# Optimization experiments

Measured on AMD Instinct MI355X. Metric: run time of the kernel, lower is better.

## Reference

```python
import jax, jax.numpy as jnp
import numpy as np

B, N, D = 2, 2048, 1024
H = 16
HD = D // H  # 64
NEG = -1e30


def setup_inputs() -> dict:
    key = jax.random.key(0)
    ks = jax.random.split(key, 6)
    s = 0.02
    return {
        "x": jax.random.normal(ks[0], (B, N, D), dtype=jnp.float32),
        "Wq": jax.random.normal(ks[1], (D, D), dtype=jnp.float32) * s,
        "Wk": jax.random.normal(ks[2], (D, D), dtype=jnp.float32) * s,
        "Wv": jax.random.normal(ks[3], (D, D), dtype=jnp.float32) * s,
        "Wo": jax.random.normal(ks[4], (D, D), dtype=jnp.float32) * s,
        "Wf": jax.random.normal(ks[5], (D, H), dtype=jnp.float32) * s,
    }


def reference(x, Wq, Wk, Wv, Wo, Wf):
    b, n, d = x.shape
    h, hd = H, HD
    scale = hd ** -0.5
    # projections (Linear without bias; weights stored as [in, out])
    q = (x @ Wq).reshape(b, n, h, hd).transpose(0, 2, 1, 3)  # b h n hd
    k = (x @ Wk).reshape(b, n, h, hd).transpose(0, 2, 1, 3)
    v = (x @ Wv).reshape(b, n, h, hd).transpose(0, 2, 1, 3)
    # per-head log forget gate, cumulative sum over positions
    log_f = jax.nn.log_sigmoid(x @ Wf).transpose(0, 2, 1)  # b h n
    c = jnp.cumsum(log_f, axis=-1)  # b h n
    # scores with additive decay bias: bias[i,j] = c[i] - c[j] (j <= i)
    scores = jnp.einsum('bhid,bhjd->bhij', q, k) * scale
    scores = scores + c[..., :, None] - c[..., None, :]
    causal = jnp.tril(jnp.ones((n, n), dtype=bool))
    scores = jnp.where(causal, scores, NEG)
    attn = jax.nn.softmax(scores, axis=-1)
    out = jnp.einsum('bhij,bhjd->bhid', attn, v)  # b h n hd
    out = out.transpose(0, 2, 1, 3).reshape(b, n, d)
    return out @ Wo
```

## Files before the change

### kernel.cpp

```cpp
#include <hip/hip_runtime.h>
#include <hip/hip_bf16.h>
#include <stdint.h>

#define NN 2048
#define DD 1024
#define HH 16
#define HDD 64
#define QBLK 64
#define KVBLK 128

typedef unsigned short u16;
typedef __attribute__((ext_vector_type(8))) __bf16 bf16x8_t;
typedef __attribute__((ext_vector_type(4))) float f32x4_t;

#define LOG2E 1.44269504f

static __device__ __forceinline__ u16 f2bf(float f) {
  union { float f; uint32_t u; } v; v.f = f;
  uint32_t r = v.u + 0x7FFFu + ((v.u >> 16) & 1u);
  return (u16)(r >> 16);
}

static __device__ __forceinline__ uint32_t packbf2(float a, float b) {
  __hip_bfloat162 h2 = __float22bfloat162_rn(make_float2(a, b));
  union { __hip_bfloat162 hh; uint32_t u; } cvt; cvt.hh = h2;
  return cvt.u;
}

static __device__ __forceinline__ float exp2_raw(float x) {
  float r;
  asm("v_exp_f32 %0, %1" : "=v"(r) : "v"(x));
  return r;
}

static __device__ __forceinline__ void async_copy16(const void* g, void* l) {
  __builtin_amdgcn_global_load_lds((const __attribute__((address_space(1))) void*)g,
                                   (__attribute__((address_space(3))) void*)l, 16, 0, 0);
}

__global__ void prep_kernel(const float* __restrict__ x, const float* __restrict__ Wf,
                            float* __restrict__ lf, u16* __restrict__ xb,
                            const float* __restrict__ W0, const float* __restrict__ W1,
                            const float* __restrict__ W2, const float* __restrict__ W3,
                            u16* __restrict__ Wt) {
  __shared__ float xs[DD];
  __shared__ float part[16][17];
  __shared__ float tile[64][65];
  int t = threadIdx.x;
  if (blockIdx.x < 4096) {
    int row = blockIdx.x;
    float4 v = *(const float4*)&x[(size_t)row * DD + t * 4];
    *(float4*)&xs[t * 4] = v;
    ushort4 o;
    o.x = f2bf(v.x); o.y = f2bf(v.y); o.z = f2bf(v.z); o.w = f2bf(v.w);
    *(ushort4*)&xb[(size_t)row * DD + t * 4] = o;
    __syncthreads();
    int h = t & 15, chunk = t >> 4;
    float s = 0.f;
#pragma unroll 8
    for (int e = 0; e < 64; e++)
      s += xs[chunk * 64 + e] * Wf[(chunk * 64 + e) * HH + h];
    part[chunk][h] = s;
    __syncthreads();
    if (t < 16) {
      float z = 0.f;
#pragma unroll
      for (int i = 0; i < 16; i++) z += part[i][t];
      float ls = fminf(z, 0.f) - log1pf(__expf(-fabsf(z)));
      int b = row >> 11, n = row & (NN - 1);
      lf[(b * HH + t) * NN + n] = ls;
    }
  } else {
    int bid = blockIdx.x - 4096;
    int wq = bid >> 8;
    const float* W = wq == 0 ? W0 : wq == 1 ? W1 : wq == 2 ? W2 : W3;
    u16* out = Wt + (size_t)wq * DD * DD;
    int bx = bid & 15;
    int by = (bid >> 4) & 15;
    int c = t & 63, r4 = t >> 6;
#pragma unroll
    for (int i = 0; i < 16; i++) {
      int row = i * 4 + r4;
      tile[row][c] = W[(by * 64 + row) * DD + bx * 64 + c];
    }
    __syncthreads();
#pragma unroll
    for (int i = 0; i < 16; i++) {
      int row = i * 4 + r4;
      out[(bx * 64 + row) * DD + by * 64 + c] = f2bf(tile[c][row]);
    }
  }
}

__global__ __launch_bounds__(512, 4) void gemm_kernel(const u16* __restrict__ A,
                                                      const u16* __restrict__ Wt,
                                                      u16* __restrict__ oQ, u16* __restrict__ oK,
                                                      u16* __restrict__ oV,
                                                      const float* __restrict__ lf,
                                                      float* __restrict__ cwp) {
  if (blockIdx.x == 24) {
    if (threadIdx.x < 64) {
      int bh = blockIdx.y;
      int lane = threadIdx.x;
      const float* in = lf + bh * NN;
      float* out = cwp + bh * NN;
      float carry = 0.f;
      for (int t0 = 0; t0 < NN; t0 += 256) {
        float4 v = *(const float4*)&in[t0 + lane * 4];
        float s1 = v.x + v.y, s2 = s1 + v.z, s3 = s2 + v.w;
        float incl = s3;
#pragma unroll
        for (int off = 1; off < 64; off <<= 1) {
          float u = __shfl_up(incl, off, 64);
          if (lane >= off) incl += u;
        }
        float excl = incl - s3 + carry;
        float4 o;
        o.x = (excl + v.x) * LOG2E; o.y = (excl + s1) * LOG2E;
        o.z = (excl + s2) * LOG2E; o.w = (excl + s3) * LOG2E;
        *(float4*)&out[t0 + lane * 4] = o;
        carry = __shfl(incl, 63, 64) + carry;
      }
    }
    return;
  }

  __shared__ u16 Als[128 * 64];
  __shared__ u16 Bls[128 * 64];
  int m0 = blockIdx.y * 128, n0 = blockIdx.x * 128;
  int tid = threadIdx.x;
  int lane = tid & 63, w = tid >> 6;
  int wm = w >> 2, wn = w & 3;
  int lr = lane & 15, lg = lane >> 4;

  const u16* gA[2]; const u16* gB[2]; u16* lA[2]; u16* lB[2];
#pragma unroll
  for (int j = 0; j < 2; j++) {
    int s = tid + j * 512;
    int row = s >> 3, ch = s & 7;
    int scol = (ch ^ (row & 7)) * 8;
    gA[j] = &A [(size_t)(m0 + row) * DD + scol];
    gB[j] = &Wt[(size_t)(n0 + row) * DD + scol];
    lA[j] = &Als[s * 8];
    lB[j] = &Bls[s * 8];
  }

  f32x4_t acc[4][2];
#pragma unroll
  for (int i = 0; i < 4; i++)
#pragma unroll
    for (int j = 0; j < 2; j++) acc[i][j] = (f32x4_t){0.f, 0.f, 0.f, 0.f};

  for (int kt = 0; kt < DD; kt += 64) {
    __syncthreads();
#pragma unroll
    for (int j = 0; j < 2; j++) {
      async_copy16(gA[j] + kt, lA[j]);
      async_copy16(gB[j] + kt, lB[j]);
    }
    __syncthreads();
#pragma unroll
    for (int kk = 0; kk < 2; kk++) {
      bf16x8_t af[4], bfv[2];
#pragma unroll
      for (int mi = 0; mi < 4; mi++) {
        int row = wm * 64 + mi * 16 + lr;
        int boff = (row * 128 + kk * 64 + lg * 16) ^ ((row & 7) << 4);
        af[mi] = *(const bf16x8_t*)((const char*)Als + boff);
      }
#pragma unroll
      for (int ni = 0; ni < 2; ni++) {
        int row = wn * 32 + ni * 16 + lr;
        int boff = (row * 128 + kk * 64 + lg * 16) ^ ((row & 7) << 4);
        bfv[ni] = *(const bf16x8_t*)((const char*)Bls + boff);
      }
#pragma unroll
      for (int mi = 0; mi < 4; mi++)
#pragma unroll
        for (int ni = 0; ni < 2; ni++)
          acc[mi][ni] = __builtin_amdgcn_mfma_f32_16x16x32_bf16(af[mi], bfv[ni], acc[mi][ni], 0, 0, 0);
    }
  }

  int which = n0 >> 10;
  int nl0 = n0 & 1023;
  if (which == 2) {
#pragma unroll
    for (int mi = 0; mi < 4; mi++)
#pragma unroll
      for (int ni = 0; ni < 2; ni++) {
        int gcol = nl0 + wn * 32 + ni * 16 + lr;
        int h = gcol >> 6, hd = gcol & 63;
        int grow0 = m0 + wm * 64 + mi * 16 + lg * 4;
        int b = grow0 >> 11, n = grow0 & (NN - 1);
        ushort4 o4;
        o4.x = f2bf(acc[mi][ni][0]);
        o4.y = f2bf(acc[mi][ni][1]);
        o4.z = f2bf(acc[mi][ni][2]);
        o4.w = f2bf(acc[mi][ni][3]);
        *(ushort4*)&oV[((size_t)(b * HH + h) * HDD + hd) * NN + n] = o4;
      }
  } else {
    u16* outp = which == 0 ? oQ : oK;
#pragma unroll
    for (int mi = 0; mi < 4; mi++)
#pragma unroll
      for (int ni = 0; ni < 2; ni++) {
        int gcol = nl0 + wn * 32 + ni * 16 + lr;
        int h = gcol >> 6, hd = gcol & 63;
#pragma unroll
        for (int r = 0; r < 4; r++) {
          int grow = m0 + wm * 64 + mi * 16 + lg * 4 + r;
          int b = grow >> 11, n = grow & (NN - 1);
          outp[((size_t)(b * HH + h) * NN + n) * HDD + hd] = f2bf(acc[mi][ni][r]);
        }
      }
  }
}

__global__ __launch_bounds__(512, 4) void gemm_out_kernel(const u16* __restrict__ A,
                                                          const u16* __restrict__ Wt,
                                                          float* __restrict__ oF) {
  __shared__ u16 Als[128 * 64];
  __shared__ u16 Bls[64 * 64];
  int m0 = blockIdx.y * 128, n0 = blockIdx.x * 64;
  int tid = threadIdx.x;
  int lane = tid & 63, w = tid >> 6;
  int wm = w >> 2, wn = w & 3;
  int lr = lane & 15, lg = lane >> 4;

  const u16* gA[2]; u16* lA[2];
#pragma unroll
  for (int j = 0; j < 2; j++) {
    int s = tid + j * 512;
    int row = s >> 3, ch = s & 7;
    int scol = (ch ^ (row & 7)) * 8;
    gA[j] = &A[(size_t)(m0 + row) * DD + scol];
    lA[j] = &Als[s * 8];
  }
  int rowb = tid >> 3, chb = tid & 7;
  const u16* gB = &Wt[(size_t)(n0 + rowb) * DD + ((chb ^ (rowb & 7)) * 8)];
  u16* lB = &Bls[tid * 8];

  f32x4_t acc[4];
#pragma unroll
  for (int i = 0; i < 4; i++) acc[i] = (f32x4_t){0.f, 0.f, 0.f, 0.f};

  for (int kt = 0; kt < DD; kt += 64) {
    __syncthreads();
#pragma unroll
    for (int j = 0; j < 2; j++) async_copy16(gA[j] + kt, lA[j]);
    async_copy16(gB + kt, lB);
    __syncthreads();
#pragma unroll
    for (int kk = 0; kk < 2; kk++) {
      bf16x8_t af[4], bf1;
#pragma unroll
      for (int mi = 0; mi < 4; mi++) {
        int row = wm * 64 + mi * 16 + lr;
        int boff = (row * 128 + kk * 64 + lg * 16) ^ ((row & 7) << 4);
        af[mi] = *(const bf16x8_t*)((const char*)Als + boff);
      }
      {
        int row = wn * 16 + lr;
        int boff = (row * 128 + kk * 64 + lg * 16) ^ ((row & 7) << 4);
        bf1 = *(const bf16x8_t*)((const char*)Bls + boff);
      }
#pragma unroll
      for (int mi = 0; mi < 4; mi++)
        acc[mi] = __builtin_amdgcn_mfma_f32_16x16x32_bf16(af[mi], bf1, acc[mi], 0, 0, 0);
    }
  }

#pragma unroll
  for (int mi = 0; mi < 4; mi++) {
    int gcol = n0 + wn * 16 + lr;
#pragma unroll
    for (int r = 0; r < 4; r++) {
      int grow = m0 + wm * 64 + mi * 16 + lg * 4 + r;
      oF[(size_t)grow * DD + gcol] = acc[mi][r];
    }
  }
}

__global__ __launch_bounds__(256) void attn_kernel(const u16* __restrict__ Q,
                                                   const u16* __restrict__ K,
                                                   const u16* __restrict__ Vt,
                                                   const float* __restrict__ cw,
                                                   u16* __restrict__ O) {
  __shared__ u16 Kls[2][KVBLK * 64];
  __shared__ u16 Vls[2][64 * KVBLK];
  int flat = blockIdx.y * gridDim.x + blockIdx.x;
  int swz = (flat & 7) * 64 + (flat >> 3);
  int pidx = swz & 15, bh = swz >> 4;
  int tid = threadIdx.x;
  int lane = tid & 63, w = tid >> 6;
  int lr = lane & 15, lg = lane >> 4;
  const u16* Qh = Q + (size_t)bh * NN * HDD;
  const u16* Kh = K + (size_t)bh * NN * HDD;
  const u16* Vh = Vt + (size_t)bh * HDD * NN;
  const float* ch = cw + bh * NN;
  int b = bh >> 4, h = bh & 15;

  const float SCL = 0.125f * LOG2E;

  const u16* gk[4]; const u16* gv[4];
#pragma unroll
  for (int j = 0; j < 4; j++) {
    int s = tid + j * 256;
    int kr = s >> 3, kc = s & 7;
    gk[j] = &Kh[(size_t)kr * HDD + ((kc ^ (kr & 7)) * 8)];
    int vr = s >> 4, vc = s & 15;
    gv[j] = &Vh[(size_t)vr * NN + ((vc ^ (vr & 7)) * 8)];
  }

  for (int which = 0; which < 2; which++) {
    int tile = which == 0 ? (31 - pidx) : pidx;
    int qb = tile * QBLK + w * 16;
    int iq = qb + lr;

    bf16x8_t qf[2];
#pragma unroll
    for (int s = 0; s < 2; s++)
      qf[s] = *(const bf16x8_t*)&Qh[(size_t)iq * HDD + s * 32 + lg * 8];
    float cq = ch[iq];

    float lsum = 0.f;
    f32x4_t oacc[4];
#pragma unroll
    for (int fn = 0; fn < 4; fn++) oacc[fn] = (f32x4_t){0.f, 0.f, 0.f, 0.f};

    int nt = (tile >> 1) + 1;

#pragma unroll
    for (int j = 0; j < 4; j++) {
      int s = tid + j * 256;
      async_copy16(gk[j], &Kls[0][s * 8]);
      async_copy16(gv[j], &Vls[0][s * 8]);
    }
    __syncthreads();

    int cur = 0;
    for (int kvt = 0; kvt < nt; kvt++) {
      if (kvt + 1 < nt) {
        size_t kvn = (size_t)(kvt + 1) * KVBLK;
        int nb = cur ^ 1;
#pragma unroll
        for (int j = 0; j < 4; j++) {
          int s = tid + j * 256;
          async_copy16(gk[j] + kvn * HDD, &Kls[nb][s * 8]);
          async_copy16(gv[j] + kvn, &Vls[nb][s * 8]);
        }
      }
      int kv0 = kvt * KVBLK;
      const u16* Kb = Kls[cur];
      const u16* Vb = Vls[cur];
      float4 ckv[8];
#pragma unroll
      for (int f = 0; f < 8; f++)
        ckv[f] = *(const float4*)&ch[kv0 + f * 16 + lg * 4];

      f32x4_t sacc[8];
#pragma unroll
      for (int f = 0; f < 8; f++) sacc[f] = (f32x4_t){0.f, 0.f, 0.f, 0.f};
      __builtin_amdgcn_s_setprio(1);
#pragma unroll
      for (int f = 0; f < 8; f++) {
        int row = f * 16 + lr;
#pragma unroll
        for (int s = 0; s < 2; s++) {
          int boff = (row * 128 + s * 64 + lg * 16) ^ ((row & 7) << 4);
          bf16x8_t kf = *(const bf16x8_t*)((const char*)Kb + boff);
          sacc[f] = __builtin_amdgcn_mfma_f32_16x16x32_bf16(kf, qf[s], sacc[f], 0, 0, 0);
        }
      }
      __builtin_amdgcn_s_setprio(0);

      bool diag = (kvt == nt - 1);
      float pv[8][4];
#pragma unroll
      for (int f = 0; f < 8; f++) {
        const float* ckp = &ckv[f].x;
#pragma unroll
        for (int r = 0; r < 4; r++) {
          float val = fmaf(sacc[f][r], SCL, cq - ckp[r]);
          float e = exp2_raw(val);
          if (diag && (kv0 + f * 16 + lg * 4 + r) > iq) e = 0.f;
          pv[f][r] = e; lsum += e;
        }
      }

      bf16x8_t pa[4];
#pragma unroll
      for (int s = 0; s < 4; s++) {
        uint32_t x0 = packbf2(pv[2 * s][0], pv[2 * s][1]);
        uint32_t x1 = packbf2(pv[2 * s][2], pv[2 * s][3]);
        uint32_t y0 = packbf2(pv[2 * s + 1][0], pv[2 * s + 1][1]);
        uint32_t y1 = packbf2(pv[2 * s + 1][2], pv[2 * s + 1][3]);
        asm volatile("v_permlane32_swap_b32 %0, %1" : "+v"(x0), "+v"(y0));
        asm volatile("v_permlane32_swap_b32 %0, %1" : "+v"(x1), "+v"(y1));
        asm volatile("v_permlane16_swap_b32 %0, %1" : "+v"(x0), "+v"(y0));
        asm volatile("v_permlane16_swap_b32 %0, %1" : "+v"(x1), "+v"(y1));
        union { uint32_t u[4]; bf16x8_t v; } pk;
        pk.u[0] = x0; pk.u[1] = x1; pk.u[2] = y0; pk.u[3] = y1;
        pa[s] = pk.v;
      }

      __builtin_amdgcn_s_setprio(1);
#pragma unroll
      for (int fn = 0; fn < 4; fn++) {
        int row = fn * 16 + lr;
#pragma unroll
        for (int s = 0; s < 4; s++) {
          int boff = row * 256 + ((s * 64 + lg * 16) ^ ((row & 7) << 4));
          bf16x8_t vf = *(const bf16x8_t*)((const char*)Vb + boff);
          oacc[fn] = __builtin_amdgcn_mfma_f32_16x16x32_bf16(vf, pa[s], oacc[fn], 0, 0, 0);
        }
      }
      __builtin_amdgcn_s_setprio(0);
      __syncthreads();
      cur ^= 1;
    }

    lsum += __shfl_xor(lsum, 16, 64);
    lsum += __shfl_xor(lsum, 32, 64);
    float rinv = 1.0f / lsum;

    u16* orow = O + ((size_t)(b * NN + iq)) * DD + h * HDD;
#pragma unroll
    for (int fn = 0; fn < 4; fn++) {
      ushort4 o4;
      o4.x = f2bf(oacc[fn][0] * rinv);
      o4.y = f2bf(oacc[fn][1] * rinv);
      o4.z = f2bf(oacc[fn][2] * rinv);
      o4.w = f2bf(oacc[fn][3] * rinv);
      *(ushort4*)&orow[fn * 16 + lg * 4] = o4;
    }
  }
}

extern "C" void kernel_launch(void* const* d_in, const int* in_sizes, int n_in,
                              void* d_out, int out_size, void* d_ws, size_t ws_size,
                              hipStream_t stream) {
  const float* x  = (const float*)d_in[0];
  const float* Wq = (const float*)d_in[1];
  const float* Wk = (const float*)d_in[2];
  const float* Wv = (const float*)d_in[3];
  const float* Wo = (const float*)d_in[4];
  const float* Wf = (const float*)d_in[5];
  float* out = (float*)d_out;
  char* ws = (char*)d_ws;
  const size_t MB = 1024 * 1024;
  u16* x_bf  = (u16*)(ws + 0);
  u16* WqkvT = (u16*)(ws + 8 * MB);
  u16* Qw    = (u16*)(ws + 16 * MB);
  u16* Kw    = (u16*)(ws + 24 * MB);
  u16* Vw    = (u16*)(ws + 32 * MB);
  u16* Ow    = (u16*)(ws + 40 * MB);
  float* lf  = (float*)(ws + 48 * MB);
  float* cwp = (float*)(ws + 48 * MB + 262144);

  prep_kernel<<<5120, 256, 0, stream>>>(x, Wf, lf, x_bf, Wq, Wk, Wv, Wo, WqkvT);
  gemm_kernel<<<dim3(25, 32), 512, 0, stream>>>(x_bf, WqkvT, Qw, Kw, Vw, lf, cwp);
  attn_kernel<<<dim3(16, 32), 256, 0, stream>>>(Qw, Kw, Vw, cwp, Ow);
  gemm_out_kernel<<<dim3(16, 32), 512, 0, stream>>>(Ow, WqkvT + (size_t)3 * DD * DD, out);
}
```

Before: 117.7 us.

## Software-pipeline QK^T of the next KV tile with softmax and PV

Restructures the attention inner loop so the QK^T MFMAs for tile k+1 are issued before the exp/softmax and PV work of tile k, with ping-pong score accumulators. V gets a triple buffer so loads can be staged two tiles ahead, while K keeps its double buffer. The aim is to overlap matrix-core work with the exp/VALU phase and to hide load latency. In exchange it raises LDS use and register pressure from the second score array, which could lower occupancy.

After: 146.9 us. 1.25x slower.

```diff
diff --git a/kernel.cpp b/kernel.cpp
--- a/kernel.cpp
+++ b/kernel.cpp
@@ -289,7 +289,7 @@
                                                    const float* __restrict__ cw,
                                                    u16* __restrict__ O) {
   __shared__ u16 Kls[2][KVBLK * 64];
-  __shared__ u16 Vls[2][64 * KVBLK];
+  __shared__ u16 Vls[3][64 * KVBLK];
   int flat = blockIdx.y * gridDim.x + blockIdx.x;
   int swz = (flat & 7) * 64 + (flat >> 3);
   int pidx = swz & 15, bh = swz >> 4;
@@ -332,37 +332,22 @@
 
     int nt = (tile >> 1) + 1;
 
-#pragma unroll
-    for (int j = 0; j < 4; j++) {
-      int s = tid + j * 256;
-      async_copy16(gk[j], &Kls[0][s * 8]);
-      async_copy16(gv[j], &Vls[0][s * 8]);
-    }
-    __syncthreads();
-
-    int cur = 0;
-    for (int kvt = 0; kvt < nt; kvt++) {
-      if (kvt + 1 < nt) {
-        size_t kvn = (size_t)(kvt + 1) * KVBLK;
-        int nb = cur ^ 1;
-#pragma unroll
-        for (int j = 0; j < 4; j++) {
-          int s = tid + j * 256;
-          async_copy16(gk[j] + kvn * HDD, &Kls[nb][s * 8]);
-          async_copy16(gv[j] + kvn, &Vls[nb][s * 8]);
-        }
-      }
-      int kv0 = kvt * KVBLK;
-      const u16* Kb = Kls[cur];
-      const u16* Vb = Vls[cur];
-      float4 ckv[8];
-#pragma unroll
-      for (int f = 0; f < 8; f++)
-        ckv[f] = *(const float4*)&ch[kv0 + f * 16 + lg * 4];
-
-      f32x4_t sacc[8];
-#pragma unroll
-      for (int f = 0; f < 8; f++) sacc[f] = (f32x4_t){0.f, 0.f, 0.f, 0.f};
+    auto stage = [&](int t) {
+      u16* kb = Kls[t & 1];
+      u16* vb = Vls[t % 3];
+      size_t kvn = (size_t)t * KVBLK;
+#pragma unroll
+      for (int j = 0; j < 4; j++) {
+        int s = tid + j * 256;
+        async_copy16(gk[j] + kvn * HDD, &kb[s * 8]);
+        async_copy16(gv[j] + kvn, &vb[s * 8]);
+      }
+    };
+
+    auto qk_compute = [&](int t, f32x4_t (&S)[8]) {
+      const u16* Kb = Kls[t & 1];
+#pragma unroll
+      for (int f = 0; f < 8; f++) S[f] = (f32x4_t){0.f, 0.f, 0.f, 0.f};
       __builtin_amdgcn_s_setprio(1);
 #pragma unroll
       for (int f = 0; f < 8; f++) {
@@ -371,19 +356,31 @@
         for (int s = 0; s < 2; s++) {
           int boff = (row * 128 + s * 64 + lg * 16) ^ ((row & 7) << 4);
           bf16x8_t kf = *(const bf16x8_t*)((const char*)Kb + boff);
-          sacc[f] = __builtin_amdgcn_mfma_f32_16x16x32_bf16(kf, qf[s], sacc[f], 0, 0, 0);
+          S[f] = __builtin_amdgcn_mfma_f32_16x16x32_bf16(kf, qf[s], S[f], 0, 0, 0);
         }
       }
       __builtin_amdgcn_s_setprio(0);
-
-      bool diag = (kvt == nt - 1);
+    };
+
+    auto iter = [&](int k, f32x4_t (&Scur)[8], f32x4_t (&Snext)[8]) {
+      __syncthreads();
+      if (k + 2 < nt) stage(k + 2);
+      if (k + 1 < nt) qk_compute(k + 1, Snext);
+
+      int kv0 = k * KVBLK;
+      float4 ckv[8];
+#pragma unroll
+      for (int f = 0; f < 8; f++)
+        ckv[f] = *(const float4*)&ch[kv0 + f * 16 + lg * 4];
+
+      bool diag = (k == nt - 1);
       float pv[8][4];
 #pragma unroll
       for (int f = 0; f < 8; f++) {
         const float* ckp = &ckv[f].x;
 #pragma unroll
         for (int r = 0; r < 4; r++) {
-          float val = fmaf(sacc[f][r], SCL, cq - ckp[r]);
+          float val = fmaf(Scur[f][r], SCL, cq - ckp[r]);
           float e = exp2_raw(val);
           if (diag && (kv0 + f * 16 + lg * 4 + r) > iq) e = 0.f;
           pv[f][r] = e; lsum += e;
@@ -406,6 +403,7 @@
         pa[s] = pk.v;
       }
 
+      const u16* Vb = Vls[k % 3];
       __builtin_amdgcn_s_setprio(1);
 #pragma unroll
       for (int fn = 0; fn < 4; fn++) {
@@ -418,9 +416,20 @@
         }
       }
       __builtin_amdgcn_s_setprio(0);
-      __syncthreads();
-      cur ^= 1;
-    }
+    };
+
+    f32x4_t sA[8], sB[8];
+    stage(0);
+    __syncthreads();
+    if (nt > 1) stage(1);
+    qk_compute(0, sA);
+
+    int k = 0;
+    while (true) {
+      iter(k, sA, sB); if (++k >= nt) break;
+      iter(k, sB, sA); if (++k >= nt) break;
+    }
+    __syncthreads();
 
     lsum += __shfl_xor(lsum, 16, 64);
     lsum += __shfl_xor(lsum, 32, 64);
```
